# Kernel tuning notes

Measured on AMD Instinct MI355X. Metric: run time of the kernel, lower is better.

The kernel has to match this reference:

```python
import jax, jax.numpy as jnp
import numpy as np

B, N, DIN, DH, H_MLP, L, C = 64, 1024, 64, 128, 128, 3, 4


def setup_inputs() -> dict:
    key = jax.random.key(0)
    ks = jax.random.split(key, 12)
    s = 0.05  # weight scale for numerical stability
    return {
        "x": jax.random.normal(ks[0], (B, N, DIN), jnp.float32),
        "U": jax.random.normal(ks[1], (3, N, N), jnp.float32) / np.sqrt(N),
        "w1_0": jax.random.normal(ks[2], (3, DIN, H_MLP), jnp.float32) * s,
        "b1_0": jnp.zeros((3, H_MLP), jnp.float32),
        "w2_0": jax.random.normal(ks[3], (3, H_MLP, DH), jnp.float32) * s,
        "b2_0": jnp.zeros((3, DH), jnp.float32),
        "w1_r": jax.random.normal(ks[4], (L - 1, 3, DH, H_MLP), jnp.float32) * s,
        "b1_r": jnp.zeros((L - 1, 3, H_MLP), jnp.float32),
        "w2_r": jax.random.normal(ks[5], (L - 1, 3, H_MLP, DH), jnp.float32) * s,
        "b2_r": jnp.zeros((L - 1, 3, DH), jnp.float32),
        "bw": jnp.ones((L, 3), jnp.float32),  # weight1/2/3 init to 1.0 per layer
        "Wc1": jax.random.normal(ks[6], (DH, 128), jnp.float32) * s,
        "bc1": jnp.zeros((128,), jnp.float32),
        "alpha": jnp.full((128,), 0.25, jnp.float32),  # PReLU init
        "Wc2": jax.random.normal(ks[7], (128, C), jnp.float32) * s,
        "bc2": jnp.zeros((C,), jnp.float32),
    }


def _gcn_multi(h, U, w1, b1, w2, b2, w3):
    """One GraphConv_multi layer: 3 spectral branches, softmax-weighted sum.
    h: [B,N,D_in], U: [3,N,N], w1:[3,Din,H], w2:[3,H,Dout], w3:[3]."""
    # agg = U^T @ h per branch (U is shared across batch; no repeat needed)
    agg = jnp.einsum('kji,bjd->kbid', U, h)                     # [3,B,N,Din]
    m = jax.nn.relu(jnp.einsum('kbid,kdh->kbih', agg, w1) + b1[:, None, None, :])
    m = jnp.einsum('kbih,kho->kbio', m, w2) + b2[:, None, None, :]  # [3,B,N,Dout]
    out = jnp.einsum('kij,kbjd->kbid', U, m)                    # U @ mlp_out
    ws = jax.nn.softmax(w3)                                     # branch mix
    return jnp.einsum('k,kbid->bid', ws, out)


def reference(x, U, w1_0, b1_0, w2_0, b2_0, w1_r, b1_r, w2_r, b2_r,
              bw, Wc1, bc1, alpha, Wc2, bc2):
    h = jax.nn.relu(_gcn_multi(x, U, w1_0, b1_0, w2_0, b2_0, bw[0]))
    for l in range(w1_r.shape[0]):  # remaining num_layers-1 GCN layers
        h = jax.nn.relu(_gcn_multi(h, U, w1_r[l], b1_r[l], w2_r[l], b2_r[l], bw[l + 1]))
    pooled = jnp.mean(h, axis=1)                                # 'mean' graph pooling
    z = pooled @ Wc1 + bc1
    z = jnp.where(z > 0, z, alpha * z)                          # PReLU(128); dropout = eval no-op
    return z @ Wc2 + bc2                                        # [B, C]
```

## Files before the change

### kernel.cpp

```cpp
#include <hip/hip_runtime.h>


typedef unsigned short u16;
typedef short bf16x8 __attribute__((ext_vector_type(8)));
typedef float f32x4 __attribute__((ext_vector_type(4)));
typedef u16 u16x4 __attribute__((ext_vector_type(4)));

__device__ __forceinline__ u16 f2bf(float x){
  unsigned u = __builtin_bit_cast(unsigned, x);
  u += 0x7fffu + ((u >> 16) & 1u);
  return (u16)(u >> 16);
}
__device__ __forceinline__ float bf2f(u16 h){
  return __builtin_bit_cast(float, ((unsigned)h) << 16);
}
__device__ __forceinline__ void gload16(const u16* g, u16* l){
  __builtin_amdgcn_global_load_lds(
      (const __attribute__((address_space(1))) unsigned int*)(g),
      (__attribute__((address_space(3))) unsigned int*)(l), 16, 0, 0);
}


__global__ void prep_weights(const float* __restrict__ w1_0, const float* __restrict__ w2_0,
                             const float* __restrict__ w1_r, const float* __restrict__ w2_r,
                             const float* __restrict__ bw,
                             u16* __restrict__ W1T0, u16* __restrict__ W2T0,
                             u16* __restrict__ W1Tr, u16* __restrict__ W2Tr,
                             float* __restrict__ wsb){
  int id = blockIdx.x*256 + threadIdx.x;
  if (id < 3){
    float a0=bw[id*3+0], a1=bw[id*3+1], a2=bw[id*3+2];
    float m = fmaxf(a0,fmaxf(a1,a2));
    float e0=expf(a0-m), e1=expf(a1-m), e2=expf(a2-m);
    float s = e0+e1+e2;
    wsb[id*3+0]=e0/s; wsb[id*3+1]=e1/s; wsb[id*3+2]=e2/s;
  }
  if (id < 24576){
    int k=id/8192, rem=id%8192, h=rem/64, d=rem%64;
    W1T0[id] = f2bf(w1_0[(k*64+d)*128 + h]);
  } else if (id < 73728){
    int t=id-24576, k=t/16384, rem=t%16384, o=rem/128, h=rem%128;
    W2T0[t] = f2bf(w2_0[(k*128+h)*128 + o]);
  } else if (id < 172032){
    int t=id-73728, lk=t/16384, rem=t%16384, h=rem/128, d=rem%128;
    W1Tr[t] = f2bf(w1_r[lk*16384 + d*128 + h]);
  } else if (id < 270336){
    int t=id-172032, lk=t/16384, rem=t%16384, o=rem/128, h=rem%128;
    W2Tr[t] = f2bf(w2_r[lk*16384 + h*128 + o]);
  }
}

__global__ void prep_U(const float* __restrict__ U, u16* __restrict__ UTcat,
                       u16* __restrict__ Ucat){
  __shared__ float t[32][33];
  int k = blockIdx.z, i0 = blockIdx.x*32, j0 = blockIdx.y*32;
  size_t kb = (size_t)k << 20;
  #pragma unroll
  for (int rr=0; rr<4; rr++){
    int r = threadIdx.y*4+rr, c = threadIdx.x;
    float v = U[kb + (size_t)(j0+r)*1024 + i0+c];
    t[r][c] = v;
    Ucat[(size_t)(j0+r)*3072 + k*1024 + i0+c] = f2bf(v);
  }
  __syncthreads();
  #pragma unroll
  for (int rr=0; rr<4; rr++){
    int r = threadIdx.y*4+rr, c = threadIdx.x;
    UTcat[kb + (size_t)(i0+r)*1024 + j0+c] = f2bf(t[c][r]);
  }
}

__global__ void prep_x(const float* __restrict__ x, u16* __restrict__ H){
  __shared__ float t[32][33];
  int b = blockIdx.z, d0 = blockIdx.x*32, j0 = blockIdx.y*32;
  #pragma unroll
  for (int rr=0;rr<4;rr++){
    int r=threadIdx.y*4+rr, c=threadIdx.x;
    t[r][c] = x[((size_t)b*1024 + j0+r)*64 + d0+c];
  }
  __syncthreads();
  #pragma unroll
  for (int rr=0;rr<4;rr++){
    int r=threadIdx.y*4+rr, c=threadIdx.x;
    H[(size_t)(b*64 + d0+r)*1024 + j0+c] = f2bf(t[c][r]);
  }
}

template<bool RELU, int REORD>
__global__ __launch_bounds__(512, 4)
void gemm_big(const u16* __restrict__ A, const u16* __restrict__ B,
              u16* __restrict__ C, int Nc, int K, long aZ, int cRowZ)
{
  __shared__ __align__(16) u16 ldsA[3*8192];
  __shared__ __align__(16) u16 ldsB[3*4096];
  const int tid = threadIdx.x;
  const int z = blockIdx.z;
  const u16* Ab = A + (size_t)z*aZ;
  const int gx = gridDim.x;
  const int nwg = gx*gridDim.y;
  int flat = blockIdx.y*gx + blockIdx.x;
  if ((nwg & 7) == 0) flat = (flat & 7)*(nwg >> 3) + (flat >> 3);
  const int bm = (flat/gx)*256, bn = (flat%gx)*128;
  const int wave = tid>>6, lane = tid&63;
  const int wm = (wave&3)*64, wn = (wave>>2)*64;
  const int rl = lane&15, ksb = lane>>4;
  const int srow = tid>>2;
  const int scol = ((tid&3)*8) ^ (((tid>>3)&3)<<3);
  const int NT = K>>5;

  f32x4 acc[4][4];
  #pragma unroll
  for (int mi=0;mi<4;mi++)
    #pragma unroll
    for (int ni=0;ni<4;ni++){ f32x4 zv={0.f,0.f,0.f,0.f}; acc[mi][ni]=zv; }

  auto stage = [&](int t){
    const int sa = (t%3)*8192, sb = (t%3)*4096;
    const int k0 = t<<5;
    #pragma unroll
    for (int c=0;c<2;c++)
      gload16(Ab + (size_t)(bm + c*128 + srow)*K + k0 + scol,
              &ldsA[sa + c*4096 + tid*8]);
    gload16(B + (size_t)(bn + srow)*K + k0 + scol, &ldsB[sb + tid*8]);
  };

  stage(0); stage(1);
  asm volatile("s_waitcnt vmcnt(3)" ::: "memory");
  __builtin_amdgcn_s_barrier();
  __builtin_amdgcn_sched_barrier(0);

  for (int t=0; t<NT; t++){
    const int sa = (t%3)*8192, sb = (t%3)*4096;
    bf16x8 af[4], bfr[4];
    #pragma unroll
    for (int mi=0;mi<4;mi++){
      const int row = wm + mi*16 + rl;
      af[mi] = *(const bf16x8*)&ldsA[sa + row*32 + ((ksb*8) ^ (((row>>1)&3)<<3))];
    }
    #pragma unroll
    for (int ni=0;ni<4;ni++){
      const int row = wn + ni*16 + rl;
      bfr[ni] = *(const bf16x8*)&ldsB[sb + row*32 + ((ksb*8) ^ (((row>>1)&3)<<3))];
    }
    if (t+2 < NT) stage(t+2);
    __builtin_amdgcn_s_setprio(1);
    #pragma unroll
    for (int ni=0;ni<4;ni++)
      #pragma unroll
      for (int mi=0;mi<4;mi++)
        acc[mi][ni] = __builtin_amdgcn_mfma_f32_16x16x32_bf16(af[mi], bfr[ni], acc[mi][ni], 0,0,0);
    __builtin_amdgcn_s_setprio(0);
    if (t+2 < NT)      asm volatile("s_waitcnt vmcnt(3)" ::: "memory");
    else if (t+1 < NT) asm volatile("s_waitcnt vmcnt(0)" ::: "memory");
    __builtin_amdgcn_s_barrier();
    __builtin_amdgcn_sched_barrier(0);
  }

  #pragma unroll
  for (int ni=0;ni<4;ni++){
    const int col = bn + wn + ni*16 + rl;
    #pragma unroll
    for (int mi=0;mi<4;mi++){
      const int row0 = bm + wm + mi*16 + ksb*4;
      #pragma unroll
      for (int r=0;r<4;r++){
        float v = acc[mi][ni][r];
        if (RELU) v = fmaxf(v, 0.f);
        if constexpr (REORD){
          const int Din = 1 << REORD;
          const int bb = col >> REORD, d = col & (Din-1);
          C[((size_t)((z<<6) + bb)*1024 + row0 + r)*Din + d] = f2bf(v);
        } else {
          C[(size_t)(z*cRowZ + row0 + r)*Nc + col] = f2bf(v);
        }
      }
    }
  }
}

template<int DIN>
__global__ __launch_bounds__(256)
void fused_mlp(const u16* __restrict__ AGG, const u16* __restrict__ W1T,
               const u16* __restrict__ W2T, const float* __restrict__ b1g,
               const float* __restrict__ b2g, const float* __restrict__ wsl,
               u16* __restrict__ M2T)
{
  constexpr int JW1 = 128*DIN;
  __shared__ __align__(16) u16 lds[2*JW1 + 16384];
  const int tid = threadIdx.x;
  const int jt = blockIdx.x, z = blockIdx.z, k = z>>6, b = z&63;
  const u16* Ag  = AGG + ((size_t)z*1024 + jt*128)*DIN;
  const u16* W1k = W1T + k*JW1;
  const u16* W2k = W2T + k*16384;
  const int wave = tid>>6, lane = tid&63;
  const int wm = (wave>>1)*64, wn = (wave&1)*64;
  const int rl = lane&15, ksb = lane>>4;
  const int xr = (rl&7)<<3;

  constexpr int CJ = JW1/2048;
  #pragma unroll
  for (int c=0;c<CJ;c++){
    const int e = c*2048 + tid*8, row = e/DIN, col = e%DIN;
    gload16(Ag + (size_t)row*DIN + (col ^ ((row&7)<<3)), &lds[e]);
  }
  #pragma unroll
  for (int c=0;c<CJ;c++){
    const int e = c*2048 + tid*8, row = e/DIN, col = e%DIN;
    gload16(W1k + (size_t)row*DIN + (col ^ ((row&7)<<3)), &lds[JW1 + e]);
  }
  #pragma unroll
  for (int c=0;c<8;c++){
    const int e = c*2048 + tid*8, row = e>>7, col = e&127;
    gload16(W2k + (size_t)row*128 + (col ^ ((row&7)<<3)), &lds[2*JW1 + e]);
  }
  asm volatile("s_waitcnt vmcnt(8)" ::: "memory");
  __builtin_amdgcn_s_barrier();
  __builtin_amdgcn_sched_barrier(0);

  f32x4 acc[4][4];
  #pragma unroll
  for (int mi=0;mi<4;mi++)
    #pragma unroll
    for (int ni=0;ni<4;ni++){ f32x4 zv={0.f,0.f,0.f,0.f}; acc[mi][ni]=zv; }
  #pragma unroll
  for (int k0=0; k0<DIN; k0+=32){
    bf16x8 aj[4], wh[4];
    #pragma unroll
    for (int mi=0;mi<4;mi++)
      aj[mi] = *(const bf16x8*)&lds[(wm+mi*16+rl)*DIN + ((k0+ksb*8) ^ xr)];
    #pragma unroll
    for (int ni=0;ni<4;ni++)
      wh[ni] = *(const bf16x8*)&lds[JW1 + (wn+ni*16+rl)*DIN + ((k0+ksb*8) ^ xr)];
    #pragma unroll
    for (int ni=0;ni<4;ni++)
      #pragma unroll
      for (int mi=0;mi<4;mi++)
        acc[mi][ni] = __builtin_amdgcn_mfma_f32_16x16x32_bf16(aj[mi], wh[ni], acc[mi][ni], 0,0,0);
  }
  __syncthreads();

  float bh[4];
  #pragma unroll
  for (int ni=0;ni<4;ni++) bh[ni] = b1g[k*128 + wn + ni*16 + rl];
  #pragma unroll
  for (int ni=0;ni<4;ni++){
    const int h = wn + ni*16 + rl;
    #pragma unroll
    for (int mi=0;mi<4;mi++){
      #pragma unroll
      for (int r=0;r<4;r++){
        const int j = wm + mi*16 + ksb*4 + r;
        const float v = fmaxf(acc[mi][ni][r] + bh[ni], 0.f);
        lds[j*128 + (h ^ ((j&7)<<3))] = f2bf(v);
      }
    }
  }
  __syncthreads();

  f32x4 acc2[4][4];
  #pragma unroll
  for (int mi=0;mi<4;mi++)
    #pragma unroll
    for (int ni=0;ni<4;ni++){ f32x4 zv={0.f,0.f,0.f,0.f}; acc2[mi][ni]=zv; }
  #pragma unroll
  for (int k0=0; k0<128; k0+=32){
    bf16x8 ao[4], mj[4];
    #pragma unroll
    for (int mi=0;mi<4;mi++)
      ao[mi] = *(const bf16x8*)&lds[2*JW1 + (wm+mi*16+rl)*128 + ((k0+ksb*8) ^ xr)];
    #pragma unroll
    for (int ni=0;ni<4;ni++)
      mj[ni] = *(const bf16x8*)&lds[(wn+ni*16+rl)*128 + ((k0+ksb*8) ^ xr)];
    #pragma unroll
    for (int ni=0;ni<4;ni++)
      #pragma unroll
      for (int mi=0;mi<4;mi++)
        acc2[mi][ni] = __builtin_amdgcn_mfma_f32_16x16x32_bf16(ao[mi], mj[ni], acc2[mi][ni], 0,0,0);
  }

  const float ws = wsl[k];
  #pragma unroll
  for (int mi=0;mi<4;mi++){
    #pragma unroll
    for (int r=0;r<4;r++){
      const int o = wm + mi*16 + ksb*4 + r;
      const float bo = b2g[k*128 + o];
      #pragma unroll
      for (int ni=0;ni<4;ni++){
        const int j = wn + ni*16 + rl;
        const float v = (acc2[mi][ni][r] + bo) * ws;
        M2T[(size_t)(b*128 + o)*3072 + k*1024 + jt*128 + j] = f2bf(v);
      }
    }
  }
}

__global__ void pool_kernel(const u16* __restrict__ H, float* __restrict__ pooled){
  const int row = blockIdx.x, t = threadIdx.x;
  u16x4 v = *(const u16x4*)(H + (size_t)row*1024 + t*4);
  float s = bf2f(v.x)+bf2f(v.y)+bf2f(v.z)+bf2f(v.w);
  for (int o2=32;o2>0;o2>>=1) s += __shfl_down(s,o2);
  __shared__ float red[4];
  if ((t&63)==0) red[t>>6]=s;
  __syncthreads();
  if (t==0) pooled[row] = (red[0]+red[1]+red[2]+red[3])*(1.f/1024.f);
}

__global__ void head_kernel(const float* __restrict__ pooled, const float* __restrict__ Wc1,
                            const float* __restrict__ bc1, const float* __restrict__ alpha,
                            const float* __restrict__ Wc2, const float* __restrict__ bc2,
                            float* __restrict__ out){
  const int b = blockIdx.x, h = threadIdx.x;
  __shared__ float p[128], zz[128];
  p[h] = pooled[b*128+h];
  __syncthreads();
  float acc = bc1[h];
  for (int d=0; d<128; d++) acc = fmaf(p[d], Wc1[d*128+h], acc);
  zz[h] = acc>0.f ? acc : alpha[h]*acc;
  __syncthreads();
  if (h<4){
    float a = bc2[h];
    for (int q=0;q<128;q++) a = fmaf(zz[q], Wc2[q*4+h], a);
    out[b*4+h]=a;
  }
}

extern "C" void kernel_launch(void* const* d_in, const int* in_sizes, int n_in,
                              void* d_out, int out_size, void* d_ws, size_t ws_size,
                              hipStream_t stream)
{
  const float* x     = (const float*)d_in[0];
  const float* U     = (const float*)d_in[1];
  const float* w1_0  = (const float*)d_in[2];
  const float* b1_0  = (const float*)d_in[3];
  const float* w2_0  = (const float*)d_in[4];
  const float* b2_0  = (const float*)d_in[5];
  const float* w1_r  = (const float*)d_in[6];
  const float* b1_r  = (const float*)d_in[7];
  const float* w2_r  = (const float*)d_in[8];
  const float* b2_r  = (const float*)d_in[9];
  const float* bw    = (const float*)d_in[10];
  const float* Wc1   = (const float*)d_in[11];
  const float* bc1   = (const float*)d_in[12];
  const float* alpha = (const float*)d_in[13];
  const float* Wc2   = (const float*)d_in[14];
  const float* bc2   = (const float*)d_in[15];
  float* out = (float*)d_out;

  char* wsp = (char*)d_ws;
  size_t off = 0;
  auto alloc = [&](size_t bytes) -> void* {
    void* p = wsp + off;
    off = (off + bytes + 255) & ~(size_t)255;
    return p;
  };
  u16* UTcat = (u16*)alloc(6291456);
  u16* Ucat  = (u16*)alloc(6291456);
  u16* W1T0  = (u16*)alloc(49152);
  u16* W2T0  = (u16*)alloc(98304);
  u16* W1Tr  = (u16*)alloc(196608);
  u16* W2Tr  = (u16*)alloc(196608);
  float* wsb = (float*)alloc(256);
  u16* HT    = (u16*)alloc(16777216);
  u16* AGG   = (u16*)alloc(50331648);
  u16* M2T   = (u16*)alloc(50331648);
  float* pooled = (float*)alloc(32768);
  if (off > ws_size) return;

  prep_weights<<<1056, 256, 0, stream>>>(w1_0,w2_0,w1_r,w2_r,bw,
      W1T0,W2T0,W1Tr,W2Tr,wsb);
  prep_U<<<dim3(32,32,3), dim3(32,8), 0, stream>>>(U, UTcat, Ucat);
  prep_x<<<dim3(2,32,64), dim3(32,8), 0, stream>>>(x, HT);

  for (int l=0; l<3; l++){
    const u16* w1t = l ? W1Tr + (size_t)(l-1)*3*16384 : W1T0;
    const u16* w2t = l ? W2Tr + (size_t)(l-1)*3*16384 : W2T0;
    const float* b1 = l ? b1_r + (l-1)*384 : b1_0;
    const float* b2 = l ? b2_r + (l-1)*384 : b2_0;

    if (l == 0)
      gemm_big<false,6><<<dim3(32, 4, 3), 512, 0, stream>>>(
          UTcat, HT, AGG, 4096, 1024, 1048576L, 0);
    else
      gemm_big<false,7><<<dim3(64, 4, 3), 512, 0, stream>>>(
          UTcat, HT, AGG, 8192, 1024, 1048576L, 0);
    if (l == 0)
      fused_mlp<64><<<dim3(8, 1, 192), 256, 0, stream>>>(
          AGG, w1t, w2t, b1, b2, wsb + l*3, M2T);
    else
      fused_mlp<128><<<dim3(8, 1, 192), 256, 0, stream>>>(
          AGG, w1t, w2t, b1, b2, wsb + l*3, M2T);
    gemm_big<true,0><<<dim3(8, 32, 1), 512, 0, stream>>>(
        M2T, Ucat, HT, 1024, 3072, 0L, 0);
  }
  pool_kernel<<<8192, 256, 0, stream>>>(HT, pooled);
  head_kernel<<<64, 128, 0, stream>>>(pooled, Wc1, bc1, alpha, Wc2, bc2, out);
}
```

Before: 450.6 us.

## Load GEMM B operand directly from global into registers, bypassing LDS

The B tile in gemm_big is no longer staged through LDS. Each wave now reads its B fragments straight from global memory into registers and double-buffers them one K-step ahead, while A keeps its three-stage LDS pipeline. This removes the B shared-memory buffer and its LDS reads, and lowers LDS footprint. In exchange, waves that share the same B columns fetch them redundantly from global/L2 with less coalesced access. The extra register buffers also raise pressure under the existing launch bounds, and the vmcnt wait counts were retuned to match.

```diff
diff --git a/kernel.cpp b/kernel.cpp
--- a/kernel.cpp
+++ b/kernel.cpp
@@ -92,7 +92,6 @@
               u16* __restrict__ C, int Nc, int K, long aZ, int cRowZ)
 {
   __shared__ __align__(16) u16 ldsA[3*8192];
-  __shared__ __align__(16) u16 ldsB[3*4096];
   const int tid = threadIdx.x;
   const int z = blockIdx.z;
   const u16* Ab = A + (size_t)z*aZ;
@@ -107,6 +106,7 @@
   const int srow = tid>>2;
   const int scol = ((tid&3)*8) ^ (((tid>>3)&3)<<3);
   const int NT = K>>5;
+  const u16* Bf = B + (size_t)(bn + wn + rl)*K + ksb*8;
 
   f32x4 acc[4][4];
   #pragma unroll
@@ -114,46 +114,54 @@
     #pragma unroll
     for (int ni=0;ni<4;ni++){ f32x4 zv={0.f,0.f,0.f,0.f}; acc[mi][ni]=zv; }
 
-  auto stage = [&](int t){
-    const int sa = (t%3)*8192, sb = (t%3)*4096;
+  auto stageA = [&](int t){
+    const int sa = (t%3)*8192;
     const int k0 = t<<5;
     #pragma unroll
     for (int c=0;c<2;c++)
       gload16(Ab + (size_t)(bm + c*128 + srow)*K + k0 + scol,
               &ldsA[sa + c*4096 + tid*8]);
-    gload16(B + (size_t)(bn + srow)*K + k0 + scol, &ldsB[sb + tid*8]);
   };
 
-  stage(0); stage(1);
-  asm volatile("s_waitcnt vmcnt(3)" ::: "memory");
+  bf16x8 bcur[4], bnext[4];
+  #pragma unroll
+  for (int ni=0;ni<4;ni++)
+    bcur[ni] = *(const bf16x8*)(Bf + (size_t)(ni*16)*K);
+  stageA(0); stageA(1);
+  asm volatile("s_waitcnt vmcnt(2)" ::: "memory");
   __builtin_amdgcn_s_barrier();
   __builtin_amdgcn_sched_barrier(0);
 
   for (int t=0; t<NT; t++){
-    const int sa = (t%3)*8192, sb = (t%3)*4096;
-    bf16x8 af[4], bfr[4];
+    const int sa = (t%3)*8192;
+    bf16x8 af[4];
     #pragma unroll
     for (int mi=0;mi<4;mi++){
       const int row = wm + mi*16 + rl;
       af[mi] = *(const bf16x8*)&ldsA[sa + row*32 + ((ksb*8) ^ (((row>>1)&3)<<3))];
     }
-    #pragma unroll
-    for (int ni=0;ni<4;ni++){
-      const int row = wn + ni*16 + rl;
-      bfr[ni] = *(const bf16x8*)&ldsB[sb + row*32 + ((ksb*8) ^ (((row>>1)&3)<<3))];
-    }
-    if (t+2 < NT) stage(t+2);
+    if (t+1 < NT){
+      const int k1 = (t+1)<<5;
+      #pragma unroll
+      for (int ni=0;ni<4;ni++)
+        bnext[ni] = *(const bf16x8*)(Bf + (size_t)(ni*16)*K + k1);
+    }
+    if (t+2 < NT) stageA(t+2);
     __builtin_amdgcn_s_setprio(1);
     #pragma unroll
     for (int ni=0;ni<4;ni++)
       #pragma unroll
       for (int mi=0;mi<4;mi++)
-        acc[mi][ni] = __builtin_amdgcn_mfma_f32_16x16x32_bf16(af[mi], bfr[ni], acc[mi][ni], 0,0,0);
+        acc[mi][ni] = __builtin_amdgcn_mfma_f32_16x16x32_bf16(af[mi], bcur[ni], acc[mi][ni], 0,0,0);
     __builtin_amdgcn_s_setprio(0);
-    if (t+2 < NT)      asm volatile("s_waitcnt vmcnt(3)" ::: "memory");
-    else if (t+1 < NT) asm volatile("s_waitcnt vmcnt(0)" ::: "memory");
-    __builtin_amdgcn_s_barrier();
-    __builtin_amdgcn_sched_barrier(0);
+    if (t+2 < NT)      asm volatile("s_waitcnt vmcnt(6)" ::: "memory");
+    else if (t+1 < NT) asm volatile("s_waitcnt vmcnt(4)" ::: "memory");
+    if (t+1 < NT){
+      __builtin_amdgcn_s_barrier();
+      __builtin_amdgcn_sched_barrier(0);
+      #pragma unroll
+      for (int ni=0;ni<4;ni++) bcur[ni] = bnext[ni];
+    }
   }
 
   #pragma unroll
```

New measurement: 1.086 ms. 141% more time.

## Fuse aggregation GEMM with per-branch MLP for layers after the first

Applied to the files above, without the earlier changes.

For layers 1 and 2, a new kernel computes the U^T·H aggregation tile and, without writing it to global memory, runs both MLP matmuls (with bias, ReLU and softmax branch weight) from LDS, then writes the result to M2T. This removes the AGG round trip (about 50 MB written and read per layer) and one kernel launch. In exchange it uses a large LDS footprint (about 136 KB per block), which with launch_bounds(512,2) may limit occupancy, and adds a serial MLP tail after the GEMM main loop.

```diff
diff --git a/kernel.cpp b/kernel.cpp
--- a/kernel.cpp
+++ b/kernel.cpp
@@ -178,6 +178,186 @@
   }
 }
 
+__global__ __launch_bounds__(512, 2)
+void gemm_agg_mlp(const u16* __restrict__ A, const u16* __restrict__ B,
+                  const u16* __restrict__ W1T, const u16* __restrict__ W2T,
+                  const float* __restrict__ b1g, const float* __restrict__ b2g,
+                  const float* __restrict__ wsl, u16* __restrict__ M2T)
+{
+  __shared__ __align__(16) u16 lds[69632];
+  const int tid = threadIdx.x;
+  const int z = blockIdx.z;
+  const int K = 1024, NT = 32;
+  const u16* Ab = A + (size_t)z*1048576;
+  const u16* W1k = W1T + z*16384;
+  const u16* W2k = W2T + z*16384;
+  const int gx = gridDim.x;
+  const int nwg = gx*gridDim.y;
+  int flat = blockIdx.y*gx + blockIdx.x;
+  if ((nwg & 7) == 0) flat = (flat & 7)*(nwg >> 3) + (flat >> 3);
+  const int bm = (flat/gx)*256, bn = (flat%gx)*128;
+  const int b = bn >> 7;
+  const int wave = tid>>6, lane = tid&63;
+  const int wm = (wave&3)*64, wn = (wave>>2)*64;
+  const int rl = lane&15, ksb = lane>>4;
+  const int xr = (rl&7)<<3;
+  const int srow = tid>>2;
+  const int scol = ((tid&3)*8) ^ (((tid>>3)&3)<<3);
+
+  f32x4 acc[4][4];
+  #pragma unroll
+  for (int mi=0;mi<4;mi++)
+    #pragma unroll
+    for (int ni=0;ni<4;ni++){ f32x4 zv={0.f,0.f,0.f,0.f}; acc[mi][ni]=zv; }
+
+  #pragma unroll
+  for (int c=0;c<4;c++){
+    const int e = c*4096 + tid*8, row = e>>7, col = e&127;
+    gload16(W1k + row*128 + (col ^ ((row&7)<<3)), &lds[36864 + e]);
+  }
+  #pragma unroll
+  for (int c=0;c<4;c++){
+    const int e = c*4096 + tid*8, row = e>>7, col = e&127;
+    gload16(W2k + row*128 + (col ^ ((row&7)<<3)), &lds[53248 + e]);
+  }
+
+  auto stage = [&](int t){
+    const int sa = (t%3)*8192, sb = 24576 + (t%3)*4096;
+    const int k0 = t<<5;
+    #pragma unroll
+    for (int c=0;c<2;c++)
+      gload16(Ab + (size_t)(bm + c*128 + srow)*K + k0 + scol,
+              &lds[sa + c*4096 + tid*8]);
+    gload16(B + (size_t)(bn + srow)*K + k0 + scol, &lds[sb + tid*8]);
+  };
+
+  stage(0); stage(1);
+  asm volatile("s_waitcnt vmcnt(3)" ::: "memory");
+  __builtin_amdgcn_s_barrier();
+  __builtin_amdgcn_sched_barrier(0);
+
+  for (int t=0; t<NT; t++){
+    const int sa = (t%3)*8192, sb = 24576 + (t%3)*4096;
+    bf16x8 af[4], bfr[4];
+    #pragma unroll
+    for (int mi=0;mi<4;mi++){
+      const int row = wm + mi*16 + rl;
+      af[mi] = *(const bf16x8*)&lds[sa + row*32 + ((ksb*8) ^ (((row>>1)&3)<<3))];
+    }
+    #pragma unroll
+    for (int ni=0;ni<4;ni++){
+      const int row = wn + ni*16 + rl;
+      bfr[ni] = *(const bf16x8*)&lds[sb + row*32 + ((ksb*8) ^ (((row>>1)&3)<<3))];
+    }
+    if (t+2 < NT) stage(t+2);
+    __builtin_amdgcn_s_setprio(1);
+    #pragma unroll
+    for (int ni=0;ni<4;ni++)
+      #pragma unroll
+      for (int mi=0;mi<4;mi++)
+        acc[mi][ni] = __builtin_amdgcn_mfma_f32_16x16x32_bf16(af[mi], bfr[ni], acc[mi][ni], 0,0,0);
+    __builtin_amdgcn_s_setprio(0);
+    if (t+2 < NT)      asm volatile("s_waitcnt vmcnt(3)" ::: "memory");
+    else if (t+1 < NT) asm volatile("s_waitcnt vmcnt(0)" ::: "memory");
+    __builtin_amdgcn_s_barrier();
+    __builtin_amdgcn_sched_barrier(0);
+  }
+
+  __syncthreads();
+  #pragma unroll
+  for (int ni=0;ni<4;ni++){
+    const int d = wn + ni*16 + rl;
+    #pragma unroll
+    for (int mi=0;mi<4;mi++){
+      #pragma unroll
+      for (int r=0;r<4;r++){
+        const int j = wm + mi*16 + ksb*4 + r;
+        lds[j*128 + (d ^ ((j&7)<<3))] = f2bf(acc[mi][ni][r]);
+      }
+    }
+  }
+  __syncthreads();
+
+  const int jg = (wave&3)*64, hg = (wave>>2)*64;
+  f32x4 acc1[4][4];
+  #pragma unroll
+  for (int mi=0;mi<4;mi++)
+    #pragma unroll
+    for (int ni=0;ni<4;ni++){ f32x4 zv={0.f,0.f,0.f,0.f}; acc1[mi][ni]=zv; }
+  #pragma unroll
+  for (int kk=0;kk<4;kk++){
+    const int k0 = kk*32;
+    bf16x8 aj[4], wh[4];
+    #pragma unroll
+    for (int mi=0;mi<4;mi++)
+      aj[mi] = *(const bf16x8*)&lds[(jg+mi*16+rl)*128 + ((k0+ksb*8) ^ xr)];
+    #pragma unroll
+    for (int ni=0;ni<4;ni++)
+      wh[ni] = *(const bf16x8*)&lds[36864 + (hg+ni*16+rl)*128 + ((k0+ksb*8) ^ xr)];
+    #pragma unroll
+    for (int ni=0;ni<4;ni++)
+      #pragma unroll
+      for (int mi=0;mi<4;mi++)
+        acc1[mi][ni] = __builtin_amdgcn_mfma_f32_16x16x32_bf16(aj[mi], wh[ni], acc1[mi][ni], 0,0,0);
+  }
+  __syncthreads();
+
+  float bh[4];
+  #pragma unroll
+  for (int ni=0;ni<4;ni++) bh[ni] = b1g[z*128 + hg + ni*16 + rl];
+  #pragma unroll
+  for (int ni=0;ni<4;ni++){
+    const int h = hg + ni*16 + rl;
+    #pragma unroll
+    for (int mi=0;mi<4;mi++){
+      #pragma unroll
+      for (int r=0;r<4;r++){
+        const int j = jg + mi*16 + ksb*4 + r;
+        lds[j*128 + (h ^ ((j&7)<<3))] = f2bf(fmaxf(acc1[mi][ni][r] + bh[ni], 0.f));
+      }
+    }
+  }
+  __syncthreads();
+
+  const int og = (wave>>2)*64, jg2 = (wave&3)*64;
+  f32x4 acc2[4][4];
+  #pragma unroll
+  for (int mi=0;mi<4;mi++)
+    #pragma unroll
+    for (int ni=0;ni<4;ni++){ f32x4 zv={0.f,0.f,0.f,0.f}; acc2[mi][ni]=zv; }
+  #pragma unroll
+  for (int kk=0;kk<4;kk++){
+    const int k0 = kk*32;
+    bf16x8 wo[4], mj[4];
+    #pragma unroll
+    for (int mi=0;mi<4;mi++)
+      wo[mi] = *(const bf16x8*)&lds[53248 + (og+mi*16+rl)*128 + ((k0+ksb*8) ^ xr)];
+    #pragma unroll
+    for (int ni=0;ni<4;ni++)
+      mj[ni] = *(const bf16x8*)&lds[(jg2+ni*16+rl)*128 + ((k0+ksb*8) ^ xr)];
+    #pragma unroll
+    for (int ni=0;ni<4;ni++)
+      #pragma unroll
+      for (int mi=0;mi<4;mi++)
+        acc2[mi][ni] = __builtin_amdgcn_mfma_f32_16x16x32_bf16(wo[mi], mj[ni], acc2[mi][ni], 0,0,0);
+  }
+
+  const float ws = wsl[z];
+  #pragma unroll
+  for (int mi=0;mi<4;mi++){
+    #pragma unroll
+    for (int r=0;r<4;r++){
+      const int o = og + mi*16 + ksb*4 + r;
+      const float bo = b2g[z*128 + o];
+      #pragma unroll
+      for (int ni=0;ni<4;ni++){
+        const int j = jg2 + ni*16 + rl;
+        M2T[(size_t)(b*128 + o)*3072 + z*1024 + bm + j] = f2bf((acc2[mi][ni][r] + bo) * ws);
+      }
+    }
+  }
+}
+
 template<int DIN>
 __global__ __launch_bounds__(256)
 void fused_mlp(const u16* __restrict__ AGG, const u16* __restrict__ W1T,
@@ -250,8 +430,7 @@
       #pragma unroll
       for (int r=0;r<4;r++){
         const int j = wm + mi*16 + ksb*4 + r;
-        const float v = fmaxf(acc[mi][ni][r] + bh[ni], 0.f);
-        lds[j*128 + (h ^ ((j&7)<<3))] = f2bf(v);
+        lds[j*128 + (h ^ ((j&7)<<3))] = f2bf(fmaxf(acc[mi][ni][r] + bh[ni], 0.f));
       }
     }
   }
@@ -288,8 +467,7 @@
       #pragma unroll
       for (int ni=0;ni<4;ni++){
         const int j = wn + ni*16 + rl;
-        const float v = (acc2[mi][ni][r] + bo) * ws;
-        M2T[(size_t)(b*128 + o)*3072 + k*1024 + jt*128 + j] = f2bf(v);
+        M2T[(size_t)(b*128 + o)*3072 + k*1024 + jt*128 + j] = f2bf((acc2[mi][ni][r] + bo) * ws);
       }
     }
   }
@@ -373,23 +551,20 @@
   prep_x<<<dim3(2,32,64), dim3(32,8), 0, stream>>>(x, HT);
 
   for (int l=0; l<3; l++){
-    const u16* w1t = l ? W1Tr + (size_t)(l-1)*3*16384 : W1T0;
-    const u16* w2t = l ? W2Tr + (size_t)(l-1)*3*16384 : W2T0;
     const float* b1 = l ? b1_r + (l-1)*384 : b1_0;
     const float* b2 = l ? b2_r + (l-1)*384 : b2_0;
 
-    if (l == 0)
+    if (l == 0){
       gemm_big<false,6><<<dim3(32, 4, 3), 512, 0, stream>>>(
           UTcat, HT, AGG, 4096, 1024, 1048576L, 0);
-    else
-      gemm_big<false,7><<<dim3(64, 4, 3), 512, 0, stream>>>(
-          UTcat, HT, AGG, 8192, 1024, 1048576L, 0);
-    if (l == 0)
       fused_mlp<64><<<dim3(8, 1, 192), 256, 0, stream>>>(
-          AGG, w1t, w2t, b1, b2, wsb + l*3, M2T);
-    else
-      fused_mlp<128><<<dim3(8, 1, 192), 256, 0, stream>>>(
-          AGG, w1t, w2t, b1, b2, wsb + l*3, M2T);
+          AGG, W1T0, W2T0, b1, b2, wsb, M2T);
+    } else {
+      gemm_agg_mlp<<<dim3(64, 4, 3), 512, 0, stream>>>(
+          UTcat, HT,
+          W1Tr + (size_t)(l-1)*3*16384, W2Tr + (size_t)(l-1)*3*16384,
+          b1, b2, wsb + l*3, M2T);
+    }
     gemm_big<true,0><<<dim3(8, 32, 1), 512, 0, stream>>>(
         M2T, Ucat, HT, 1024, 3072, 0L, 0);
   }
```

Measured after the change: 413.0 us. 1.09x faster.
